# Kernel optimization log

Measured on AMD Instinct MI355X. Metric: run time of the kernel, lower is better.

The kernel has to match this reference:

```python
import jax, jax.numpy as jnp
import numpy as np

D_MODEL = 512
TEMP = 30.0  # softmax temperature used by TransformerTrack-style RelationUnit
EPS = 1e-5
NORM_SCALE = float(np.sqrt(1.0 / (D_MODEL * 4 * 4)))


def _instance_l2norm(x):
    # x: [n, hw, b, d]; InstanceL2Norm over (dim, h, w) per (image, batch) sample
    n, hw, b, d = x.shape
    ss = jnp.sum(x * x, axis=(1, 3), keepdims=True)  # [n,1,b,1]
    return x * (NORM_SCALE * jnp.sqrt((d * hw) / (ss + EPS)))


def _cnorm(r, i):
    # joint L2 normalization of a complex vector along last axis
    s = jnp.sqrt(jnp.sum(r * r + i * i, axis=-1, keepdims=True) + 1e-12)
    return r / s, i / s


def _rel_self_attn(xr, xi, er, ei, WK):
    # xr/xi: [n, L, b, d]; er/ei: [n, L, L, b, dk] relative (helix) embeddings
    qr, qi = _cnorm(xr @ WK, xi @ WK)           # [n,L,b,dk]
    # real part of complex conjugate inner product <q, k>
    scores = (jnp.einsum('nqbk,nlbk->nbql', qr, qr)
              + jnp.einsum('nqbk,nlbk->nbql', qi, qi)
              + jnp.einsum('nqbk,nqlbk->nbql', qr, er)
              + jnp.einsum('nqbk,nqlbk->nbql', qi, ei))
    A = jax.nn.softmax(scores * TEMP, axis=-1)  # [n,b,q,l]
    out_r = jnp.einsum('nbql,nlbd->nqbd', A, xr)
    out_i = jnp.einsum('nbql,nlbd->nqbd', A, xi)
    return out_r, out_i


def _cross_attn(qr_in, qi_in, kr_in, ki_in, vr, vi, WK):
    # q: [Lq,b,d]; k,v: [Lk,b,d]
    qr, qi = _cnorm(qr_in @ WK, qi_in @ WK)
    kr, ki = _cnorm(kr_in @ WK, ki_in @ WK)
    scores = jnp.einsum('qbk,lbk->bql', qr, kr) + jnp.einsum('qbk,lbk->bql', qi, ki)
    A = jax.nn.softmax(scores * TEMP, axis=-1)
    out_r = jnp.einsum('bql,lbd->qbd', A, vr)
    out_i = jnp.einsum('bql,lbd->qbd', A, vi)
    return out_r, out_i


def _forward(src_real, src_imag, tgt_real, tgt_imag,
             src_emb_real, src_emb_imag, tgt_emb_real, tgt_emb_imag,
             pos_real, pos_imag, WK_rel, WK_cross):
    n, b, d, h, w = src_real.shape
    hw = h * w

    def tok(x):  # [n,b,d,h,w] -> [n,hw,b,d]
        return x.reshape(n, b, d, hw).transpose(0, 3, 1, 2)

    def emb(x):  # [n,b,dk,hw,hw] -> [n,hw,hw,b,dk]
        return x.transpose(0, 3, 4, 1, 2)

    sr, si = tok(src_real), tok(src_imag)
    tr, ti = tok(tgt_real), tok(tgt_imag)
    esr, esi = emb(src_emb_real), emb(src_emb_imag)
    etr, eti = emb(tgt_emb_real), emb(tgt_emb_imag)

    # ---- encoder (num_layers = 1) ----
    s2r, s2i = _rel_self_attn(sr, si, esr, esi, WK_rel)
    mem_r = _instance_l2norm(sr + s2r).reshape(n * hw, b, d)
    mem_i = _instance_l2norm(si + s2i).reshape(n * hw, b, d)

    # pos: [n,b,h,w] -> [n*hw, b, d] (broadcast over dim as in .repeat(1,1,dim))
    pr = jnp.broadcast_to(pos_real.reshape(n, b, hw).transpose(0, 2, 1).reshape(n * hw, b, 1), (n * hw, b, d))
    pi = jnp.broadcast_to(pos_imag.reshape(n, b, hw).transpose(0, 2, 1).reshape(n * hw, b, 1), (n * hw, b, d))

    def IN3(x):
        return _instance_l2norm(x.reshape(n, hw, b, d)).reshape(n * hw, b, d)

    # ---- decoder (num_layers = 1) ----
    t2r, t2i = _rel_self_attn(tr, ti, etr, eti, WK_rel)
    xr = _instance_l2norm(tr + t2r).reshape(n * hw, b, d)
    xi = _instance_l2norm(ti + t2i).reshape(n * hw, b, d)

    mask_r, mask_i = _cross_attn(xr, xi, mem_r, mem_i, pr, pi, WK_cross)
    y2r = IN3(xr * mask_r)
    y2i = IN3(xi * mask_i)

    t3r, t3i = _cross_attn(xr, xi, mem_r, mem_i, mem_r * pr, mem_i * pi, WK_cross)
    y4r = IN3(xr + t3r)
    y4i = IN3(xi + t3i)

    out_r = IN3(y2r + y4r)
    out_i = IN3(y2i + y4i)

    feat_r = out_r.reshape(n, h, w, b, d).transpose(0, 3, 4, 1, 2).reshape(n * b, d, h, w)
    feat_i = out_i.reshape(n, h, w, b, d).transpose(0, 3, 4, 1, 2).reshape(n * b, d, h, w)
    return out_r, out_i, feat_r, feat_i


def setup_inputs() -> dict:
    key = jax.random.key(0)
    ks = jax.random.split(key, 12)
    n, b, d, h, dk = 2, 2, 512, 16, 64
    hw = h * h
    inp = {
        'src_real': jax.random.normal(ks[0], (n, b, d, h, h), jnp.float32),
        'src_imag': jax.random.normal(ks[1], (n, b, d, h, h), jnp.float32),
        'tgt_real': jax.random.normal(ks[2], (n, b, d, h, h), jnp.float32),
        'tgt_imag': jax.random.normal(ks[3], (n, b, d, h, h), jnp.float32),
        'src_emb_real': jax.random.normal(ks[4], (n, b, dk, hw, hw), jnp.float32),
        'src_emb_imag': jax.random.normal(ks[5], (n, b, dk, hw, hw), jnp.float32),
        'tgt_emb_real': jax.random.normal(ks[6], (n, b, dk, hw, hw), jnp.float32),
        'tgt_emb_imag': jax.random.normal(ks[7], (n, b, dk, hw, hw), jnp.float32),
        'pos_real': jax.random.uniform(ks[8], (n, b, h, h), jnp.float32),
        'pos_imag': jax.random.uniform(ks[9], (n, b, h, h), jnp.float32),
        'WK_rel': jax.random.normal(ks[10], (d, dk), jnp.float32) * 0.02,
        'WK_cross': jax.random.normal(ks[11], (d, 128), jnp.float32) * 0.02,
    }
    return inp


def reference(src_real, src_imag, tgt_real, tgt_imag,
              src_emb_real, src_emb_imag, tgt_emb_real, tgt_emb_imag,
              pos_real, pos_imag, WK_rel, WK_cross):
    return _forward(src_real, src_imag, tgt_real, tgt_imag,
                    src_emb_real, src_emb_imag, tgt_emb_real, tgt_emb_imag,
                    pos_real, pos_imag, WK_rel, WK_cross)
```

## Files before the change

### kernel.cpp

```cpp
#include <hip/hip_runtime.h>
#include <cstdint>
#include <cstddef>

#define N_ 2
#define B_ 2
#define D_ 512
#define HW_ 256
#define DK_ 64
#define DKC_ 128
#define G_ 4
#define NBLK_ 32

typedef float f4 __attribute__((ext_vector_type(4)));

constexpr size_t OFF_TSR = 0;
constexpr size_t OFF_TSI = 524288;
constexpr size_t OFF_TTR = 1048576;
constexpr size_t OFF_TTI = 1572864;
constexpr size_t OFF_QSR = 2097152;
constexpr size_t OFF_QSI = OFF_QSR + 65536;
constexpr size_t OFF_QTR = OFF_QSI + 65536;
constexpr size_t OFF_QTI = OFF_QTR + 65536;
constexpr size_t OFF_AS  = OFF_QTI + 65536;
constexpr size_t OFF_AT  = OFF_AS + 262144;
constexpr size_t OFF_YSR = OFF_AT + 262144;
constexpr size_t OFF_YSI = OFF_YSR + 524288;
constexpr size_t OFF_YTR = OFF_YSI + 524288;
constexpr size_t OFF_YTI = OFF_YTR + 524288;
constexpr size_t OFF_QCR = OFF_YTI + 524288;
constexpr size_t OFF_QCI = OFF_QCR + 131072;
constexpr size_t OFF_KCR = OFF_QCI + 131072;
constexpr size_t OFF_KCI = OFF_KCR + 131072;
constexpr size_t OFF_AC  = OFF_KCI + 131072;
constexpr size_t OFF_T3R = OFF_AC + 524288;
constexpr size_t OFF_T3I = OFF_T3R + 524288;
constexpr size_t OFF_MR  = OFF_T3I + 524288;
constexpr size_t OFF_MI  = OFF_MR + 1024;
constexpr size_t OFF_P1  = OFF_MI + 1024;
constexpr size_t OFF_P2  = OFF_P1 + 1024;
constexpr size_t OFF_P3  = OFF_P2 + 512;

template<int NT>
__device__ __forceinline__ float blk_sum(float v, float* sh) {
  int tid = threadIdx.x;
  sh[tid] = v; __syncthreads();
  #pragma unroll
  for (int s = NT/2; s > 0; s >>= 1) { if (tid < s) sh[tid] += sh[tid+s]; __syncthreads(); }
  float r = sh[0]; __syncthreads(); return r;
}
template<int NT>
__device__ __forceinline__ float blk_max(float v, float* sh) {
  int tid = threadIdx.x;
  sh[tid] = v; __syncthreads();
  #pragma unroll
  for (int s = NT/2; s > 0; s >>= 1) { if (tid < s) sh[tid] = fmaxf(sh[tid], sh[tid+s]); __syncthreads(); }
  float r = sh[0]; __syncthreads(); return r;
}
__device__ __forceinline__ float wave_sum32(float v) {
  #pragma unroll
  for (int o = 16; o; o >>= 1) v += __shfl_xor(v, o, 64);
  return v;
}
__device__ __forceinline__ float wave_sum64(float v) {
  #pragma unroll
  for (int o = 32; o; o >>= 1) v += __shfl_xor(v, o, 64);
  return v;
}
__device__ __forceinline__ float wave_max64(float v) {
  #pragma unroll
  for (int o = 32; o; o >>= 1) v = fmaxf(v, __shfl_xor(v, o, 64));
  return v;
}
__device__ __forceinline__ float scale_from(const float* part, int q) {
  float ss = 0.f;
  #pragma unroll
  for (int j = 0; j < NBLK_; ++j) ss += part[q*NBLK_ + j];
  return 4.f * rsqrtf(ss + 1e-5f);
}
__device__ __forceinline__ float scale_from64(const float* part, int q) {
  float ss = 0.f;
  #pragma unroll
  for (int j = 0; j < 64; ++j) ss += part[q*64 + j];
  return 4.f * rsqrtf(ss + 1e-5f);
}
__device__ __forceinline__ void gload16(const float* g, float* l) {
  __builtin_amdgcn_global_load_lds((const __attribute__((address_space(1))) void*)g,
                                   (__attribute__((address_space(3))) void*)l, 16, 0, 0);
}

__global__ void k_transpose(const float* sR, const float* sI, const float* tR, const float* tI, float* ws) {
  int which = blockIdx.y;
  const float* in = (which==0)? sR : (which==1)? sI : (which==2)? tR : tI;
  float* out = ws + ((which==0)? OFF_TSR : (which==1)? OFF_TSI : (which==2)? OFF_TTR : OFF_TTI);
  int bx = blockIdx.x;
  int pt = bx & 3, dt = (bx>>2)&7, nb = bx>>5;
  int ni = nb>>1, bi = nb&1;
  __shared__ float tile[64][65];
  int tid = threadIdx.x;
  int p0 = pt*64, d0 = dt*64;
  #pragma unroll
  for (int it=0; it<16; ++it) {
    int i = it*256 + tid; int row = i>>6, col = i&63;
    tile[row][col] = in[(size_t)(nb*D_ + d0+row)*HW_ + p0+col];
  }
  __syncthreads();
  #pragma unroll
  for (int it=0; it<16; ++it) {
    int i = it*256 + tid; int row = i>>6, col = i&63;
    out[(size_t)((ni*HW_ + p0+row)*B_ + bi)*D_ + d0+col] = tile[col][row];
  }
}

__global__ void __launch_bounds__(256) k_qrel(float* ws, const float* WK) {
  int bx = blockIdx.x;
  int rg = bx & 127, which = bx >> 7;
  const float* Tr = ws + (which ? OFF_TTR : OFF_TSR);
  const float* Ti = ws + (which ? OFF_TTI : OFF_TSI);
  float* Qr = ws + (which ? OFF_QTR : OFF_QSR);
  float* Qi = ws + (which ? OFF_QTI : OFF_QSI);
  int R0 = rg*8;
  __shared__ float Xr[8][512], Xi[8][512];
  int tid = threadIdx.x;
  const float4* tr4 = (const float4*)(Tr + (size_t)R0*D_);
  const float4* ti4 = (const float4*)(Ti + (size_t)R0*D_);
  #pragma unroll
  for (int it=0; it<4; ++it) {
    int i = it*256 + tid;
    ((float4*)&Xr[0][0])[i] = tr4[i];
    ((float4*)&Xi[0][0])[i] = ti4[i];
  }
  __syncthreads();
  int row = tid >> 5, col2 = (tid & 31)*2;
  float a0r=0.f, a0i=0.f, a1r=0.f, a1i=0.f;
  #pragma unroll 4
  for (int d=0; d<512; ++d) {
    float2 w = *(const float2*)&WK[(size_t)d*DK_ + col2];
    float xr = Xr[row][d], xi = Xi[row][d];
    a0r += xr*w.x; a1r += xr*w.y;
    a0i += xi*w.x; a1i += xi*w.y;
  }
  float ss = wave_sum32(a0r*a0r + a1r*a1r + a0i*a0i + a1i*a1i);
  float inv = 1.f / sqrtf(ss + 1e-12f);
  size_t o = (size_t)(R0+row)*DK_ + col2;
  Qr[o]   = a0r*inv; Qr[o+1] = a1r*inv;
  Qi[o]   = a0i*inv; Qi[o+1] = a1i*inv;
}

__global__ void __launch_bounds__(128) k_gram(float* ws) {
  int bx = blockIdx.x;
  int lt = bx & 3, qt = (bx>>2)&7, nb = (bx>>5)&3, which = bx>>7;
  int ni = nb>>1, bi = nb&1;
  const float* Qr = ws + (which ? OFF_QTR : OFF_QSR);
  const float* Qi = ws + (which ? OFF_QTI : OFF_QSI);
  float* A = ws + (which ? OFF_AT : OFF_AS) + (size_t)nb*65536;
  __shared__ float Qrs[32][33], Qis[32][33], Krs[32][68], Kis[32][68];
  int tid = threadIdx.x, ty = tid>>4, tx = tid&15;
  int ty4 = ty*4, tx4 = tx*4;
  float acc[4][4] = {};
  for (int c = 0; c < 2; ++c) {
    #pragma unroll
    for (int it = 0; it < 8; ++it) {
      int i = it*128 + tid; int row = i>>5, col = i&31;
      size_t qa = (size_t)((ni*HW_ + qt*32+row)*B_ + bi)*DK_ + c*32 + col;
      Qrs[row][col] = Qr[qa];
      Qis[row][col] = Qi[qa];
    }
    #pragma unroll
    for (int it = 0; it < 16; ++it) {
      int i = it*128 + tid; int kk = i&31, col = i>>5;
      size_t ka = (size_t)((ni*HW_ + lt*64+col)*B_ + bi)*DK_ + c*32 + kk;
      Krs[kk][col] = Qr[ka];
      Kis[kk][col] = Qi[ka];
    }
    __syncthreads();
    #pragma unroll
    for (int kk = 0; kk < 32; ++kk) {
      float4 kr = *(const float4*)&Krs[kk][tx4];
      float4 ki = *(const float4*)&Kis[kk][tx4];
      #pragma unroll
      for (int i = 0; i < 4; ++i) {
        float qr = Qrs[ty4+i][kk], qi = Qis[ty4+i][kk];
        acc[i][0] += qr*kr.x + qi*ki.x;
        acc[i][1] += qr*kr.y + qi*ki.y;
        acc[i][2] += qr*kr.z + qi*ki.z;
        acc[i][3] += qr*kr.w + qi*ki.w;
      }
    }
    __syncthreads();
  }
  #pragma unroll
  for (int i = 0; i < 4; ++i)
    #pragma unroll
    for (int j = 0; j < 4; ++j)
      A[(size_t)(qt*32+ty4+i)*256 + lt*64+tx4+j] = acc[i][j];
}

__global__ void __launch_bounds__(256, 2) k_selfattn(float* ws, const float* esr, const float* esi,
                                                     const float* etr, const float* eti) {
  __shared__ float ring[4][8][2][256];
  int idx = blockIdx.x;
  int iqt = idx & 63, nb = (idx>>6)&3, which = idx>>8;
  int ni = nb>>1, bi = nb&1;
  const float* Qr = ws + (which ? OFF_QTR : OFF_QSR);
  const float* Qi = ws + (which ? OFF_QTI : OFF_QSI);
  const float* er = which ? etr : esr;
  const float* ei = which ? eti : esi;
  int tid = threadIdx.x, w = tid>>6, lane = tid&63;
  int iq = iqt*4 + w;
  float* Arow = ws + (which ? OFF_AT : OFF_AS) + (size_t)nb*65536 + (size_t)iq*256;
  int tokq = ni*HW_ + iq;
  float qvr = Qr[(size_t)(tokq*B_ + bi)*DK_ + lane];
  float qvi = Qi[(size_t)(tokq*B_ + bi)*DK_ + lane];
  const float* gr = er + (size_t)nb*4194304 + (size_t)iq*256 + lane*4;
  const float* gi = ei + (size_t)nb*4194304 + (size_t)iq*256 + lane*4;
  unsigned ldsb = (unsigned)(size_t)(__attribute__((address_space(3))) char*)&ring[w][0][0][0]
                + (unsigned)lane*16u;
  #pragma unroll
  for (int s = 0; s < 8; ++s) {
    gload16(gr + (size_t)s*65536, &ring[w][s][0][0]);
    gload16(gi + (size_t)s*65536, &ring[w][s][1][0]);
  }
  float a0=0.f, a1=0.f, a2=0.f, a3=0.f;
#define STEP(u, GSTR, KK, DOISS)                                              \
  { asm volatile("s_waitcnt vmcnt(" GSTR ")" ::: "memory");                   \
    __builtin_amdgcn_sched_barrier(0);                                        \
    f4 Rv, Iv;                                                                \
    asm volatile("ds_read_b128 %0, %2\n\tds_read_b128 %1, %2 offset:1024"     \
                 : "=v"(Rv), "=v"(Iv) : "v"(ldsb + (u)*2048u) : "memory");    \
    asm volatile("s_waitcnt lgkmcnt(0)" ::: "memory");                        \
    __builtin_amdgcn_sched_barrier(0);                                        \
    if (DOISS) {                                                              \
      gload16(gr + (size_t)((KK)+8)*65536, &ring[w][u][0][0]);                \
      gload16(gi + (size_t)((KK)+8)*65536, &ring[w][u][1][0]);                \
    }                                                                         \
    float fr = __shfl(qvr, (KK)), fi = __shfl(qvi, (KK));                     \
    a0 += fr*Rv[0] + fi*Iv[0];                                                \
    a1 += fr*Rv[1] + fi*Iv[1];                                                \
    a2 += fr*Rv[2] + fi*Iv[2];                                                \
    a3 += fr*Rv[3] + fi*Iv[3];                                                \
  }
  for (int kb = 0; kb < 56; kb += 8) {
    STEP(0, "14", kb+0, true)
    STEP(1, "14", kb+1, true)
    STEP(2, "14", kb+2, true)
    STEP(3, "14", kb+3, true)
    STEP(4, "14", kb+4, true)
    STEP(5, "14", kb+5, true)
    STEP(6, "14", kb+6, true)
    STEP(7, "14", kb+7, true)
  }
  STEP(0, "14", 56, false)
  STEP(1, "12", 57, false)
  STEP(2, "10", 58, false)
  STEP(3, "8",  59, false)
  STEP(4, "6",  60, false)
  STEP(5, "4",  61, false)
  STEP(6, "2",  62, false)
  STEP(7, "0",  63, false)
#undef STEP
  int l0 = lane*4;
  float4 g = *(const float4*)&Arow[l0];
  float s0=(a0+g.x)*30.f, s1=(a1+g.y)*30.f, s2=(a2+g.z)*30.f, s3=(a3+g.w)*30.f;
  float m = wave_max64(fmaxf(fmaxf(s0,s1), fmaxf(s2,s3)));
  float e0=__expf(s0-m), e1=__expf(s1-m), e2=__expf(s2-m), e3=__expf(s3-m);
  float inv = 1.f / wave_sum64(e0+e1+e2+e3);
  *(float4*)&Arow[l0] = make_float4(e0*inv, e1*inv, e2*inv, e3*inv);
}

__global__ void __launch_bounds__(128) k_selfapply(float* ws) {
  int bx = blockIdx.x;
  int dt = bx & 7, qt = (bx>>3)&7, nb = (bx>>6)&3, which = bx>>8;
  int ni = nb>>1, bi = nb&1;
  const float* A  = ws + (which ? OFF_AT : OFF_AS) + (size_t)nb*65536;
  const float* Xr = ws + (which ? OFF_TTR : OFF_TSR);
  const float* Xi = ws + (which ? OFF_TTI : OFF_TSI);
  float* Yr = ws + (which ? OFF_YTR : OFF_YSR);
  float* Yi = ws + (which ? OFF_YTI : OFF_YSI);
  __shared__ float As[32][33], Xrs[32][68], Xis[32][68];
  __shared__ float red[128];
  int tid = threadIdx.x, ty = tid>>4, tx = tid&15;
  int ty4 = ty*4, tx4 = tx*4;
  float ar[4][4] = {}, ai[4][4] = {};
  for (int c = 0; c < 8; ++c) {
    #pragma unroll
    for (int it = 0; it < 8; ++it) {
      int i = it*128 + tid; int row = i>>5, col = i&31;
      As[row][col] = A[(size_t)(qt*32+row)*256 + c*32+col];
    }
    #pragma unroll
    for (int it = 0; it < 16; ++it) {
      int i = it*128 + tid; int row = i>>6, col = i&63;
      size_t xb = (size_t)((ni*HW_ + c*32+row)*B_ + bi)*D_ + dt*64+col;
      Xrs[row][col] = Xr[xb]; Xis[row][col] = Xi[xb];
    }
    __syncthreads();
    #pragma unroll
    for (int kk = 0; kk < 32; ++kk) {
      float4 vr = *(const float4*)&Xrs[kk][tx4];
      float4 vi = *(const float4*)&Xis[kk][tx4];
      #pragma unroll
      for (int i = 0; i < 4; ++i) {
        float a = As[ty4+i][kk];
        ar[i][0] += a*vr.x; ar[i][1] += a*vr.y; ar[i][2] += a*vr.z; ar[i][3] += a*vr.w;
        ai[i][0] += a*vi.x; ai[i][1] += a*vi.y; ai[i][2] += a*vi.z; ai[i][3] += a*vi.w;
      }
    }
    __syncthreads();
  }
  float ssr = 0.f, ssi = 0.f;
  #pragma unroll
  for (int i = 0; i < 4; ++i) {
    size_t o = (size_t)((ni*HW_ + qt*32 + ty4+i)*B_ + bi)*D_ + dt*64 + tx4;
    #pragma unroll
    for (int j = 0; j < 4; ++j) {
      float yr = Xr[o+j] + ar[i][j];
      float yi = Xi[o+j] + ai[i][j];
      Yr[o+j] = yr; Yi[o+j] = yi;
      ssr += yr*yr; ssi += yi*yi;
    }
  }
  float tr_ = blk_sum<128>(ssr, red);
  float ti_ = blk_sum<128>(ssi, red);
  if (tid == 0) {
    ws[OFF_P1 + (size_t)((which*2+0)*G_ + nb)*64 + qt*8 + dt] = tr_;
    ws[OFF_P1 + (size_t)((which*2+1)*G_ + nb)*64 + qt*8 + dt] = ti_;
  }
}

__global__ void __launch_bounds__(256) k_crossproj(float* ws, const float* W) {
  int bx = blockIdx.x;
  int rg = bx & 127, isK = bx >> 7;
  const float* inR = ws + (isK ? OFF_YSR : OFF_YTR);
  const float* inI = ws + (isK ? OFF_YSI : OFF_YTI);
  float* oR = ws + (isK ? OFF_KCR : OFF_QCR);
  float* oI = ws + (isK ? OFF_KCI : OFF_QCI);
  int R0 = rg*8;
  __shared__ float Xr[8][512], Xi[8][512];
  int tid = threadIdx.x;
  const float4* xr4 = (const float4*)(inR + (size_t)R0*D_);
  const float4* xi4 = (const float4*)(inI + (size_t)R0*D_);
  #pragma unroll
  for (int it=0; it<4; ++it) {
    int i = it*256 + tid;
    ((float4*)&Xr[0][0])[i] = xr4[i];
    ((float4*)&Xi[0][0])[i] = xi4[i];
  }
  __syncthreads();
  int row = tid >> 5, col4 = (tid & 31)*4;
  float ar[4]={}, ai[4]={};
  #pragma unroll 4
  for (int d=0; d<512; ++d) {
    float4 w = *(const float4*)&W[(size_t)d*DKC_ + col4];
    float xr = Xr[row][d], xi = Xi[row][d];
    ar[0] += xr*w.x; ar[1] += xr*w.y; ar[2] += xr*w.z; ar[3] += xr*w.w;
    ai[0] += xi*w.x; ai[1] += xi*w.y; ai[2] += xi*w.z; ai[3] += xi*w.w;
  }
  int rr = R0 + row;
  int bi = rr & 1, gg = ((rr>>1)>>8)*2 + bi;
  float sR = scale_from64(ws + OFF_P1, (isK?0:2)*G_ + gg);
  float sI = scale_from64(ws + OFF_P1, (isK?1:3)*G_ + gg);
  ar[0]*=sR; ar[1]*=sR; ar[2]*=sR; ar[3]*=sR;
  ai[0]*=sI; ai[1]*=sI; ai[2]*=sI; ai[3]*=sI;
  float ps = ar[0]*ar[0]+ar[1]*ar[1]+ar[2]*ar[2]+ar[3]*ar[3]
           + ai[0]*ai[0]+ai[1]*ai[1]+ai[2]*ai[2]+ai[3]*ai[3];
  float ss = wave_sum32(ps);
  float inv = 1.f / sqrtf(ss + 1e-12f);
  size_t o = (size_t)rr*DKC_ + col4;
  oR[o]   = ar[0]*inv; oR[o+1] = ar[1]*inv; oR[o+2] = ar[2]*inv; oR[o+3] = ar[3]*inv;
  oI[o]   = ai[0]*inv; oI[o+1] = ai[1]*inv; oI[o+2] = ai[2]*inv; oI[o+3] = ai[3]*inv;
}

__global__ void __launch_bounds__(128) k_crossscore(float* ws) {
  int bx = blockIdx.x;
  int lt = bx & 7, qt = (bx>>3)&15, bi = bx>>7;
  const float* Qr = ws + OFF_QCR; const float* Qi = ws + OFF_QCI;
  const float* Kr = ws + OFF_KCR; const float* Ki = ws + OFF_KCI;
  float* S = ws + OFF_AC + (size_t)bi*262144;
  __shared__ float Qrs[32][33], Qis[32][33], Krs[32][68], Kis[32][68];
  int tid = threadIdx.x, ty = tid>>4, tx = tid&15;
  int ty4 = ty*4, tx4 = tx*4;
  float acc[4][4] = {};
  for (int c = 0; c < 4; ++c) {
    #pragma unroll
    for (int it = 0; it < 8; ++it) {
      int i = it*128 + tid; int row = i>>5, col = i&31;
      Qrs[row][col] = Qr[(size_t)((qt*32+row)*B_ + bi)*DKC_ + c*32 + col];
      Qis[row][col] = Qi[(size_t)((qt*32+row)*B_ + bi)*DKC_ + c*32 + col];
    }
    #pragma unroll
    for (int it = 0; it < 16; ++it) {
      int i = it*128 + tid; int kk = i&31, col = i>>5;
      Krs[kk][col] = Kr[(size_t)((lt*64+col)*B_ + bi)*DKC_ + c*32 + kk];
      Kis[kk][col] = Ki[(size_t)((lt*64+col)*B_ + bi)*DKC_ + c*32 + kk];
    }
    __syncthreads();
    #pragma unroll
    for (int kk = 0; kk < 32; ++kk) {
      float4 kr = *(const float4*)&Krs[kk][tx4];
      float4 ki = *(const float4*)&Kis[kk][tx4];
      #pragma unroll
      for (int i = 0; i < 4; ++i) {
        float qr = Qrs[ty4+i][kk], qi = Qis[ty4+i][kk];
        acc[i][0] += qr*kr.x + qi*ki.x;
        acc[i][1] += qr*kr.y + qi*ki.y;
        acc[i][2] += qr*kr.z + qi*ki.z;
        acc[i][3] += qr*kr.w + qi*ki.w;
      }
    }
    __syncthreads();
  }
  #pragma unroll
  for (int i = 0; i < 4; ++i)
    #pragma unroll
    for (int j = 0; j < 4; ++j)
      S[(size_t)(qt*32+ty4+i)*512 + lt*64+tx4+j] = acc[i][j];
}

__global__ void k_softmaxrow(float* ws, const float* posr, const float* posi) {
  int bx = blockIdx.x;
  int bi = bx >> 9, iq = bx & 511;
  float* row = ws + OFF_AC + (size_t)bi*262144 + (size_t)iq*512;
  int tid = threadIdx.x;
  float s0 = row[tid]*30.f, s1 = row[tid+256]*30.f;
  __shared__ float sh[256];
  float m = blk_max<256>(fmaxf(s0, s1), sh);
  float e0 = __expf(s0 - m), e1 = __expf(s1 - m);
  float sum = blk_sum<256>(e0 + e1, sh);
  float inv = 1.f / sum;
  float a0 = e0*inv, a1 = e1*inv;
  row[tid] = a0; row[tid+256] = a1;
  float pr0 = posr[bi*HW_ + tid],        pr1 = posr[(B_+bi)*HW_ + tid];
  float pi0 = posi[bi*HW_ + tid],        pi1 = posi[(B_+bi)*HW_ + tid];
  float mr = blk_sum<256>(a0*pr0 + a1*pr1, sh);
  float mi = blk_sum<256>(a0*pi0 + a1*pi1, sh);
  if (!tid) { ws[OFF_MR + bi*512 + iq] = mr; ws[OFF_MI + bi*512 + iq] = mi; }
}

__global__ void __launch_bounds__(128) k_crossapply(float* ws, const float* posr, const float* posi) {
  int bx = blockIdx.x;
  int dt = bx & 7, qt = (bx>>3)&15, bi = (bx>>7)&1, kc = bx>>8;
  const float* A  = ws + OFF_AC + (size_t)bi*262144;
  const float* Mr = ws + OFF_YSR; const float* Mi = ws + OFF_YSI;
  float* Pr = ws + (kc ? OFF_TSR : OFF_T3R);
  float* Pi = ws + (kc ? OFF_TSI : OFF_T3I);
  float smr = scale_from64(ws + OFF_P1, 0*G_ + kc*2 + bi);
  float smi = scale_from64(ws + OFF_P1, 1*G_ + kc*2 + bi);
  __shared__ float As[32][33], Vrs[32][68], Vis[32][68];
  int tid = threadIdx.x, ty = tid>>4, tx = tid&15;
  int ty4 = ty*4, tx4 = tx*4;
  float ar[4][4] = {}, ai[4][4] = {};
  for (int c = 0; c < 8; ++c) {
    int kb = kc*256 + c*32;
    #pragma unroll
    for (int it = 0; it < 8; ++it) {
      int i = it*128 + tid; int row = i>>5, col = i&31;
      As[row][col] = A[(size_t)(qt*32+row)*512 + kb+col];
    }
    #pragma unroll
    for (int it = 0; it < 16; ++it) {
      int i = it*128 + tid; int row = i>>6, col = i&63;
      int l = kb + row; int pl = l & 255;
      float pvr = posr[(kc*B_ + bi)*HW_ + pl] * smr;
      float pvi = posi[(kc*B_ + bi)*HW_ + pl] * smi;
      size_t vb = (size_t)(l*B_ + bi)*D_ + dt*64+col;
      Vrs[row][col] = Mr[vb] * pvr;
      Vis[row][col] = Mi[vb] * pvi;
    }
    __syncthreads();
    #pragma unroll
    for (int kk = 0; kk < 32; ++kk) {
      float4 vr = *(const float4*)&Vrs[kk][tx4];
      float4 vi = *(const float4*)&Vis[kk][tx4];
      #pragma unroll
      for (int i = 0; i < 4; ++i) {
        float a = As[ty4+i][kk];
        ar[i][0] += a*vr.x; ar[i][1] += a*vr.y; ar[i][2] += a*vr.z; ar[i][3] += a*vr.w;
        ai[i][0] += a*vi.x; ai[i][1] += a*vi.y; ai[i][2] += a*vi.z; ai[i][3] += a*vi.w;
      }
    }
    __syncthreads();
  }
  #pragma unroll
  for (int i = 0; i < 4; ++i) {
    size_t o = (size_t)((qt*32+ty4+i)*B_ + bi)*D_ + dt*64 + tx4;
    #pragma unroll
    for (int j = 0; j < 4; ++j) { Pr[o+j] = ar[i][j]; Pi[o+j] = ai[i][j]; }
  }
}

__global__ void k_reducey24(float* ws) {
  int qy = blockIdx.y;
  int g = blockIdx.x / NBLK_, blk = blockIdx.x % NBLK_;
  int ni = g>>1, bi = g&1;
  const float* X   = ws + ((qy==0 || qy==2) ? OFF_YTR : OFF_YTI);
  const float* T3a = ws + ((qy==2) ? OFF_T3R : OFF_T3I);
  const float* T3b = ws + ((qy==2) ? OFF_TSR : OFF_TSI);
  const float* M   = ws + ((qy==0) ? OFF_MR : OFF_MI);
  float sx = scale_from64(ws + OFF_P1, ((qy==0||qy==2) ? 2 : 3)*G_ + g);
  int tid = threadIdx.x;
  float acc = 0.f;
  for (int p = blk; p < HW_; p += NBLK_) {
    int l = ni*HW_ + p;
    size_t rb = (size_t)(l*B_ + bi)*D_;
    if (qy < 2) {
      float m = M[bi*512 + l] * sx;
      for (int d = tid; d < D_; d += 256) { float v = X[rb+d]*m; acc += v*v; }
    } else {
      for (int d = tid; d < D_; d += 256) { float v = X[rb+d]*sx + T3a[rb+d] + T3b[rb+d]; acc += v*v; }
    }
  }
  __shared__ float sh[256];
  float s = blk_sum<256>(acc, sh);
  if (!tid) ws[OFF_P2 + (size_t)(qy*G_ + g)*NBLK_ + blk] = s;
}

__global__ void k_combine(float* ws) {
  int y = blockIdx.y;
  int g = blockIdx.x / NBLK_, blk = blockIdx.x % NBLK_;
  int ni = g>>1, bi = g&1;
  const float* X   = ws + (y ? OFF_YTI : OFF_YTR);
  float* T3a       = ws + (y ? OFF_T3I : OFF_T3R);
  const float* T3b = ws + (y ? OFF_TSI : OFF_TSR);
  const float* M   = ws + (y ? OFF_MI : OFF_MR);
  float sx = scale_from64(ws + OFF_P1, (2+y)*G_ + g);
  float a2 = scale_from(ws + OFF_P2, y*G_ + g);
  float a4 = scale_from(ws + OFF_P2, (2+y)*G_ + g);
  int tid = threadIdx.x;
  float acc = 0.f;
  for (int p = blk; p < HW_; p += NBLK_) {
    int l = ni*HW_ + p;
    float m = M[bi*512 + l];
    size_t rb = (size_t)(l*B_ + bi)*D_;
    for (int d = tid; d < D_; d += 256) {
      float x = X[rb+d] * sx;
      float z = a2*(x*m) + a4*(x + T3a[rb+d] + T3b[rb+d]);
      T3a[rb+d] = z;
      acc += z*z;
    }
  }
  __shared__ float sh[256];
  float s = blk_sum<256>(acc, sh);
  if (!tid) ws[OFF_P3 + (size_t)(y*G_ + g)*NBLK_ + blk] = s;
}

__global__ void k_final(float* ws, float* out) {
  int y = blockIdx.y;
  int bx = blockIdx.x;
  int pt = bx & 3, dt = (bx>>2)&7, nb = bx>>5;
  int ni = nb>>1, bi = nb&1;
  const float* Z = ws + (y ? OFF_T3I : OFF_T3R);
  float s = scale_from(ws + OFF_P3, y*G_ + nb);
  float* o1 = out + (size_t)y*524288;
  float* o2 = out + (size_t)(2+y)*524288;
  __shared__ float tile[64][65];
  int tid = threadIdx.x;
  int p0 = pt*64, d0 = dt*64;
  #pragma unroll
  for (int it = 0; it < 16; ++it) {
    int i = it*256 + tid; int row = i>>6, col = i&63;
    size_t idx = (size_t)((ni*HW_ + p0+row)*B_ + bi)*D_ + d0+col;
    float v = Z[idx] * s;
    o1[idx] = v;
    tile[row][col] = v;
  }
  __syncthreads();
  #pragma unroll
  for (int it = 0; it < 16; ++it) {
    int i = it*256 + tid; int row = i>>6, col = i&63;
    o2[(size_t)(nb*D_ + d0+row)*HW_ + p0+col] = tile[col][row];
  }
}

extern "C" void kernel_launch(void* const* d_in, const int* in_sizes, int n_in,
                              void* d_out, int out_size, void* d_ws, size_t ws_size,
                              hipStream_t stream) {
  const float* srcR = (const float*)d_in[0];
  const float* srcI = (const float*)d_in[1];
  const float* tgtR = (const float*)d_in[2];
  const float* tgtI = (const float*)d_in[3];
  const float* esr  = (const float*)d_in[4];
  const float* esi  = (const float*)d_in[5];
  const float* etr  = (const float*)d_in[6];
  const float* eti  = (const float*)d_in[7];
  const float* posR = (const float*)d_in[8];
  const float* posI = (const float*)d_in[9];
  const float* WKrel   = (const float*)d_in[10];
  const float* WKcross = (const float*)d_in[11];
  float* ws  = (float*)d_ws;
  float* out = (float*)d_out;

  k_transpose <<<dim3(128,4), 256, 0, stream>>>(srcR, srcI, tgtR, tgtI, ws);
  k_qrel      <<<256, 256, 0, stream>>>(ws, WKrel);
  k_gram      <<<256, 128, 0, stream>>>(ws);
  k_selfattn  <<<512, 256, 0, stream>>>(ws, esr, esi, etr, eti);
  k_selfapply <<<512, 128, 0, stream>>>(ws);
  k_crossproj <<<256, 256, 0, stream>>>(ws, WKcross);
  k_crossscore<<<256, 128, 0, stream>>>(ws);
  k_softmaxrow<<<1024, 256, 0, stream>>>(ws, posR, posI);
  k_crossapply<<<512, 128, 0, stream>>>(ws, posR, posI);
  k_reducey24 <<<dim3(G_*NBLK_,4), 256, 0, stream>>>(ws);
  k_combine   <<<dim3(G_*NBLK_,2), 256, 0, stream>>>(ws);
  k_final     <<<dim3(128,2), 256, 0, stream>>>(ws, out);
}
```

Measured before the change: 292.6 us.

## Split relative-embedding self-attention into k-chunked partial kernel plus softmax kernel

Replaces the single-wave-per-query self-attention kernel, which streamed embeddings through an LDS ring via async global-to-LDS loads, with a kernel that splits the 64-dim k reduction into 4 chunks. Each block handles 32 queries and 16 k values using plain float4 register loads, and writes partial scores into the Y scratch region. A separate softmax kernel then sums the partials with the Gram scores and normalizes each row using block reductions. The aim is a simpler, more coalesced streaming pattern over the large embedding tensors, at the cost of an extra launch and extra partial-score traffic. Reusing the Y buffer as scratch relies on selfapply writing Y only afterward.

After: 329.4 us. 1.13x slower.

```diff
diff --git a/kernel.cpp b/kernel.cpp
--- a/kernel.cpp
+++ b/kernel.cpp
@@ -10,8 +10,6 @@
 #define DKC_ 128
 #define G_ 4
 #define NBLK_ 32
-
-typedef float f4 __attribute__((ext_vector_type(4)));
 
 constexpr size_t OFF_TSR = 0;
 constexpr size_t OFF_TSI = 524288;
@@ -61,16 +59,6 @@
   for (int o = 16; o; o >>= 1) v += __shfl_xor(v, o, 64);
   return v;
 }
-__device__ __forceinline__ float wave_sum64(float v) {
-  #pragma unroll
-  for (int o = 32; o; o >>= 1) v += __shfl_xor(v, o, 64);
-  return v;
-}
-__device__ __forceinline__ float wave_max64(float v) {
-  #pragma unroll
-  for (int o = 32; o; o >>= 1) v = fmaxf(v, __shfl_xor(v, o, 64));
-  return v;
-}
 __device__ __forceinline__ float scale_from(const float* part, int q) {
   float ss = 0.f;
   #pragma unroll
@@ -82,10 +70,6 @@
   #pragma unroll
   for (int j = 0; j < 64; ++j) ss += part[q*64 + j];
   return 4.f * rsqrtf(ss + 1e-5f);
-}
-__device__ __forceinline__ void gload16(const float* g, float* l) {
-  __builtin_amdgcn_global_load_lds((const __attribute__((address_space(1))) void*)g,
-                                   (__attribute__((address_space(3))) void*)l, 16, 0, 0);
 }
 
 __global__ void k_transpose(const float* sR, const float* sI, const float* tR, const float* tI, float* ws) {
@@ -195,76 +179,71 @@
       A[(size_t)(qt*32+ty4+i)*256 + lt*64+tx4+j] = acc[i][j];
 }
 
-__global__ void __launch_bounds__(256, 2) k_selfattn(float* ws, const float* esr, const float* esi,
-                                                     const float* etr, const float* eti) {
-  __shared__ float ring[4][8][2][256];
-  int idx = blockIdx.x;
-  int iqt = idx & 63, nb = (idx>>6)&3, which = idx>>8;
+__global__ void __launch_bounds__(256) k_selfattn_part(float* ws, const float* esr, const float* esi,
+                                                       const float* etr, const float* eti) {
+  int bx = blockIdx.x;
+  int kc = bx & 3, iqh = (bx>>2)&7, nb = (bx>>5)&3, which = bx>>7;
   int ni = nb>>1, bi = nb&1;
+  const float* er = which ? etr : esr;
+  const float* ei = which ? eti : esi;
   const float* Qr = ws + (which ? OFF_QTR : OFF_QSR);
   const float* Qi = ws + (which ? OFF_QTI : OFF_QSI);
-  const float* er = which ? etr : esr;
-  const float* ei = which ? eti : esi;
-  int tid = threadIdx.x, w = tid>>6, lane = tid&63;
-  int iq = iqt*4 + w;
+  int tid = threadIdx.x, w = tid>>6;
+  int iq0 = iqh*32, k0 = kc*16;
+  __shared__ float sQr[32][16], sQi[32][16];
+  #pragma unroll
+  for (int it=0; it<2; ++it) {
+    int j = it*256 + tid;
+    int riq = j>>4, rk = j&15;
+    int tok = ni*HW_ + iq0 + riq;
+    sQr[riq][rk] = Qr[(size_t)(tok*B_ + bi)*DK_ + k0 + rk];
+    sQi[riq][rk] = Qi[(size_t)(tok*B_ + bi)*DK_ + k0 + rk];
+  }
+  __syncthreads();
+  float4 acc[8];
+  #pragma unroll
+  for (int p=0;p<8;++p) acc[p] = make_float4(0.f,0.f,0.f,0.f);
+  const float* erb = er + ((size_t)nb*64 + k0)*65536 + (size_t)iq0*256;
+  const float* eib = ei + ((size_t)nb*64 + k0)*65536 + (size_t)iq0*256;
+  for (int k = 0; k < 16; ++k) {
+    const float4* e4r = (const float4*)(erb + (size_t)k*65536);
+    const float4* e4i = (const float4*)(eib + (size_t)k*65536);
+    float4 R[8], I[8];
+    #pragma unroll
+    for (int p=0;p<8;++p) R[p] = e4r[p*256 + tid];
+    #pragma unroll
+    for (int p=0;p<8;++p) I[p] = e4i[p*256 + tid];
+    #pragma unroll
+    for (int p=0;p<8;++p) {
+      int riq = p*4 + w;
+      float fr = sQr[riq][k], fi = sQi[riq][k];
+      acc[p].x += fr*R[p].x + fi*I[p].x;
+      acc[p].y += fr*R[p].y + fi*I[p].y;
+      acc[p].z += fr*R[p].z + fi*I[p].z;
+      acc[p].w += fr*R[p].w + fi*I[p].w;
+    }
+  }
+  float* P = ws + OFF_YSR + (((size_t)kc*2 + which)*4 + nb)*65536 + (size_t)iq0*256;
+  #pragma unroll
+  for (int p=0;p<8;++p) *(float4*)&P[(size_t)p*1024 + tid*4] = acc[p];
+}
+
+__global__ void __launch_bounds__(256) k_sm(float* ws) {
+  int bx = blockIdx.x;
+  int iq = bx & 255, nb = (bx>>8)&3, which = bx>>10;
   float* Arow = ws + (which ? OFF_AT : OFF_AS) + (size_t)nb*65536 + (size_t)iq*256;
-  int tokq = ni*HW_ + iq;
-  float qvr = Qr[(size_t)(tokq*B_ + bi)*DK_ + lane];
-  float qvi = Qi[(size_t)(tokq*B_ + bi)*DK_ + lane];
-  const float* gr = er + (size_t)nb*4194304 + (size_t)iq*256 + lane*4;
-  const float* gi = ei + (size_t)nb*4194304 + (size_t)iq*256 + lane*4;
-  unsigned ldsb = (unsigned)(size_t)(__attribute__((address_space(3))) char*)&ring[w][0][0][0]
-                + (unsigned)lane*16u;
-  #pragma unroll
-  for (int s = 0; s < 8; ++s) {
-    gload16(gr + (size_t)s*65536, &ring[w][s][0][0]);
-    gload16(gi + (size_t)s*65536, &ring[w][s][1][0]);
-  }
-  float a0=0.f, a1=0.f, a2=0.f, a3=0.f;
-#define STEP(u, GSTR, KK, DOISS)                                              \
-  { asm volatile("s_waitcnt vmcnt(" GSTR ")" ::: "memory");                   \
-    __builtin_amdgcn_sched_barrier(0);                                        \
-    f4 Rv, Iv;                                                                \
-    asm volatile("ds_read_b128 %0, %2\n\tds_read_b128 %1, %2 offset:1024"     \
-                 : "=v"(Rv), "=v"(Iv) : "v"(ldsb + (u)*2048u) : "memory");    \
-    asm volatile("s_waitcnt lgkmcnt(0)" ::: "memory");                        \
-    __builtin_amdgcn_sched_barrier(0);                                        \
-    if (DOISS) {                                                              \
-      gload16(gr + (size_t)((KK)+8)*65536, &ring[w][u][0][0]);                \
-      gload16(gi + (size_t)((KK)+8)*65536, &ring[w][u][1][0]);                \
-    }                                                                         \
-    float fr = __shfl(qvr, (KK)), fi = __shfl(qvi, (KK));                     \
-    a0 += fr*Rv[0] + fi*Iv[0];                                                \
-    a1 += fr*Rv[1] + fi*Iv[1];                                                \
-    a2 += fr*Rv[2] + fi*Iv[2];                                                \
-    a3 += fr*Rv[3] + fi*Iv[3];                                                \
-  }
-  for (int kb = 0; kb < 56; kb += 8) {
-    STEP(0, "14", kb+0, true)
-    STEP(1, "14", kb+1, true)
-    STEP(2, "14", kb+2, true)
-    STEP(3, "14", kb+3, true)
-    STEP(4, "14", kb+4, true)
-    STEP(5, "14", kb+5, true)
-    STEP(6, "14", kb+6, true)
-    STEP(7, "14", kb+7, true)
-  }
-  STEP(0, "14", 56, false)
-  STEP(1, "12", 57, false)
-  STEP(2, "10", 58, false)
-  STEP(3, "8",  59, false)
-  STEP(4, "6",  60, false)
-  STEP(5, "4",  61, false)
-  STEP(6, "2",  62, false)
-  STEP(7, "0",  63, false)
-#undef STEP
-  int l0 = lane*4;
-  float4 g = *(const float4*)&Arow[l0];
-  float s0=(a0+g.x)*30.f, s1=(a1+g.y)*30.f, s2=(a2+g.z)*30.f, s3=(a3+g.w)*30.f;
-  float m = wave_max64(fmaxf(fmaxf(s0,s1), fmaxf(s2,s3)));
-  float e0=__expf(s0-m), e1=__expf(s1-m), e2=__expf(s2-m), e3=__expf(s3-m);
-  float inv = 1.f / wave_sum64(e0+e1+e2+e3);
-  *(float4*)&Arow[l0] = make_float4(e0*inv, e1*inv, e2*inv, e3*inv);
+  const float* P = ws + OFF_YSR;
+  int tid = threadIdx.x;
+  float s = Arow[tid];
+  #pragma unroll
+  for (int kc = 0; kc < 4; ++kc)
+    s += P[(((size_t)kc*2 + which)*4 + nb)*65536 + (size_t)iq*256 + tid];
+  s *= 30.f;
+  __shared__ float sh[256];
+  float m = blk_max<256>(s, sh);
+  float e = __expf(s - m);
+  float sum = blk_sum<256>(e, sh);
+  Arow[tid] = e / sum;
 }
 
 __global__ void __launch_bounds__(128) k_selfapply(float* ws) {
@@ -589,16 +568,17 @@
   float* ws  = (float*)d_ws;
   float* out = (float*)d_out;
 
-  k_transpose <<<dim3(128,4), 256, 0, stream>>>(srcR, srcI, tgtR, tgtI, ws);
-  k_qrel      <<<256, 256, 0, stream>>>(ws, WKrel);
-  k_gram      <<<256, 128, 0, stream>>>(ws);
-  k_selfattn  <<<512, 256, 0, stream>>>(ws, esr, esi, etr, eti);
-  k_selfapply <<<512, 128, 0, stream>>>(ws);
-  k_crossproj <<<256, 256, 0, stream>>>(ws, WKcross);
-  k_crossscore<<<256, 128, 0, stream>>>(ws);
-  k_softmaxrow<<<1024, 256, 0, stream>>>(ws, posR, posI);
-  k_crossapply<<<512, 128, 0, stream>>>(ws, posR, posI);
-  k_reducey24 <<<dim3(G_*NBLK_,4), 256, 0, stream>>>(ws);
-  k_combine   <<<dim3(G_*NBLK_,2), 256, 0, stream>>>(ws);
-  k_final     <<<dim3(128,2), 256, 0, stream>>>(ws, out);
-}
+  k_transpose    <<<dim3(128,4), 256, 0, stream>>>(srcR, srcI, tgtR, tgtI, ws);
+  k_qrel         <<<256, 256, 0, stream>>>(ws, WKrel);
+  k_gram         <<<256, 128, 0, stream>>>(ws);
+  k_selfattn_part<<<256, 256, 0, stream>>>(ws, esr, esi, etr, eti);
+  k_sm           <<<2048, 256, 0, stream>>>(ws);
+  k_selfapply    <<<512, 128, 0, stream>>>(ws);
+  k_crossproj    <<<256, 256, 0, stream>>>(ws, WKcross);
+  k_crossscore   <<<256, 128, 0, stream>>>(ws);
+  k_softmaxrow   <<<1024, 256, 0, stream>>>(ws, posR, posI);
+  k_crossapply   <<<512, 128, 0, stream>>>(ws, posR, posI);
+  k_reducey24    <<<dim3(G_*NBLK_,4), 256, 0, stream>>>(ws);
+  k_combine      <<<dim3(G_*NBLK_,2), 256, 0, stream>>>(ws);
+  k_final        <<<dim3(128,2), 256, 0, stream>>>(ws, out);
+}
```
